# Kernel tuning notes

Measured on AMD Instinct MI355X. Metric: run time of the kernel, lower is better.

## Reference

```python
import math
import jax, jax.numpy as jnp
import numpy as np

FS = 16000          # sample rate implied by undefined global `fs` in source
NFFT = 320          # win_len == frame_len
HOP = 160           # inc
C_SOUND = 340.0
ARRAY_DIS = 0.027


def _steering(F, n_ch, angle_deg):
    # h = conj(exp(-1j*2*pi*f_k * sensor * d * sin(theta)/c)) -> exp(+1j*...)
    f_k = np.arange(F) * (FS // NFFT)                      # integer bins * 50 Hz
    delay = np.arange(n_ch) * ARRAY_DIS * np.sin(angle_deg * np.pi / 180.0) / C_SOUND
    h = np.exp(1j * 2.0 * np.pi * f_k[:, None] * delay[None, :]).astype(np.complex64)
    return jnp.asarray(h)[..., None]                       # [F, C, 1]


def _stft(x, window):
    # x: [B, C, L] float32; torch.stft defaults: center=True, reflect pad
    pad = NFFT // 2
    xp = jnp.pad(x, ((0, 0), (0, 0), (pad, pad)), mode='reflect')
    T = 1 + (xp.shape[-1] - NFFT) // HOP
    idx = jnp.arange(T)[:, None] * HOP + jnp.arange(NFFT)[None, :]
    frames = xp[:, :, idx] * window                        # [B, C, T, NFFT]
    return jnp.fft.rfft(frames, axis=-1)                   # [B, C, T, F] complex64


def _istft(S):
    # S: [B, F, T] complex; torch.istft with default (rectangular) window
    frames = jnp.fft.irfft(jnp.moveaxis(S, 1, 2), n=NFFT, axis=-1)  # [B, T, NFFT]
    B, T, _ = frames.shape
    out_len = NFFT + HOP * (T - 1)
    idx = jnp.arange(T)[:, None] * HOP + jnp.arange(NFFT)[None, :]
    out = jnp.zeros((B, out_len), frames.dtype).at[:, idx].add(frames)
    wsum = jnp.zeros((out_len,), frames.dtype).at[idx.reshape(-1)].add(1.0)
    pad = NFFT // 2
    return (out / wsum)[:, pad:-pad]


def setup_inputs() -> dict:
    key = jax.random.key(0)
    B, L, C = 8, 160000, 4
    mc_wav = jax.random.normal(key, (B, L, C), dtype=jnp.float32)
    # torch.kaiser_window(320, periodic=True, beta=6)
    window = jnp.asarray(np.kaiser(NFFT + 1, 6.0)[:NFFT].astype(np.float32))
    return {"mc_wav": mc_wav, "window": window}


def reference(mc_wav, window):
    B, L, C = mc_wav.shape
    # pre-normalize: remove DC per channel, scale by per-batch global max-abs
    x = mc_wav - jnp.mean(mc_wav, axis=1, keepdims=True)
    x = x / jnp.max(jnp.abs(x), axis=(1, 2), keepdims=True)
    x = jnp.transpose(x, (0, 2, 1))                        # [B, C, L]

    S = _stft(x, window)                                   # [B, C, T, F]
    F = S.shape[-1]
    Xs = jnp.transpose(S, (2, 0, 3, 1))                    # [T, B, F, C] frames-first
    T = Xs.shape[0]

    h1 = _steering(F, C, -40.0)                            # [F, C, 1]
    h2 = _steering(F, C, 40.0)
    eye = jnp.eye(C, dtype=S.dtype)

    def beam(invR, h, X):
        num = jnp.einsum('bfcd,fdo->bfco', invR, h)        # invR @ h  [B,F,C,1]
        den = jnp.einsum('fco,bfco->bf', h.conj(), num)    # h^H invR h
        w = num[..., 0] / den[..., None]                   # [B, F, C]
        return jnp.einsum('bfc,bfc->bf', w.conj(), X)      # w^H X

    def step(RXX, inp):
        X, first = inp                                     # X: [B, F, C]
        outer = jnp.einsum('bfc,bfd->bfcd', X, X.conj())
        RXX = jnp.where(first, outer, 0.05 * RXX + 0.95 * outer)
        tr = jnp.trace(RXX, axis1=-2, axis2=-1)[..., None, None]
        invR = jnp.linalg.inv(RXX + (tr / C) * eye)        # diag-loaded inverse
        return RXX, (beam(invR, h1, X), beam(invR, h2, X))

    RXX0 = jnp.zeros((B, F, C, C), dtype=S.dtype)
    firsts = jnp.arange(T) == 0
    _, (s1, s2) = jax.lax.scan(step, RXX0, (Xs, firsts))

    S1 = jnp.transpose(s1, (1, 2, 0))                      # [B, F, T]
    S2 = jnp.transpose(s2, (1, 2, 0))
    return _istft(S1), _istft(S2)
```

## Files before the change

kernel.cpp:

```cpp
#include <hip/hip_runtime.h>
#include <hip/hip_bf16.h>
#include <math.h>

#define BB 8
#define LL 160000
#define CC 4
#define NFFT 320
#define HOP 160
#define FB 161
#define TT 1001
#define TP 1024
#define RBLK 128
#define PI_D 3.14159265358979323846
#define NPAD 160320

#define CH 2
#define SCH 504
#define KWARM 4

#define GM 16016
#define KSEC 352
#define LDK 704
#define KT 11

typedef __attribute__((ext_vector_type(8))) short bf16x8;
typedef __attribute__((ext_vector_type(4))) float f32x4;

__device__ __forceinline__ float2 cmulf(float2 a, float2 b){
    return make_float2(a.x*b.x - a.y*b.y, a.x*b.y + a.y*b.x);
}
__device__ __forceinline__ float2 cmulcj(float2 a, float2 b){
    return make_float2(a.x*b.x + a.y*b.y, a.y*b.x - a.x*b.y);
}
__device__ __forceinline__ float2 cjmul(float2 a, float2 b){
    return make_float2(a.x*b.x + a.y*b.y, a.x*b.y - a.y*b.x);
}
__device__ __forceinline__ float2 csub(float2 a, float2 b){ return make_float2(a.x-b.x, a.y-b.y); }
__device__ __forceinline__ float2 cscale(float2 a, float s){ return make_float2(a.x*s, a.y*s); }
__device__ __forceinline__ float2 cdivf(float2 a, float2 b){
    float inv = 1.0f/(b.x*b.x + b.y*b.y);
    return make_float2((a.x*b.x + a.y*b.y)*inv, (a.y*b.x - a.x*b.y)*inv);
}
__device__ __forceinline__ short bf_hi(float v){
    __hip_bfloat16 h = __float2bfloat16(v);
    short s; __builtin_memcpy(&s, &h, 2); return s;
}
__device__ __forceinline__ short bf_lo(float v){
    __hip_bfloat16 h = __float2bfloat16(v);
    float r = v - __bfloat162float(h);
    __hip_bfloat16 l = __float2bfloat16(r);
    short s; __builtin_memcpy(&s, &l, 2); return s;
}

__global__ void k_gen(const float* __restrict__ win, float* __restrict__ htab,
                      short* __restrict__ Bts, short* __restrict__ Bt){
    int gid = blockIdx.x*256 + threadIdx.x;
    if (gid < 2*FB*CC){
        int i = gid;
        int c = i & 3;
        int k = (i >> 2) % FB;
        int m = i / (FB*CC);
        double coef = 2.0*PI_D*50.0*0.027*sin(40.0*PI_D/180.0)/340.0;
        double sgn = (m == 0) ? -1.0 : 1.0;
        double ph = sgn*coef*(double)k*(double)c;
        double s, c2;
        sincos(ph, &s, &c2);
        ((float2*)htab)[i] = make_float2((float)c2, (float)s);
        return;
    }
    gid -= 2*FB*CC;
    if (gid < 384*640){
        int col = gid / 640, kk = gid % 640;
        int n = (kk >= 320) ? kk - 320 : kk;
        int sec = (kk >= 320) ? 1 : 0;
        float v = 0.f;
        if (col < 2*FB){
            int k = col >> 1;
            double th = 2.0*PI_D*(double)k*(double)n/320.0;
            double s, co; sincos(th, &s, &co);
            double tw = (col & 1) ? -s : co;
            v = (float)((double)win[n]*tw);
        }
        Bts[gid] = sec ? bf_lo(v) : bf_hi(v);
        return;
    }
    gid -= 384*640;
    if (gid < NFFT*LDK){
        int n = gid / LDK, kk = gid % LDK;
        int sec = (kk >= KSEC) ? 1 : 0;
        int kk2 = kk - (sec ? KSEC : 0);
        float v = 0.f;
        if (kk2 < 2*FB){
            int bin = kk2 >> 1;
            double c = ((bin == 0 || bin == 160) ? 1.0 : 2.0) / 320.0;
            double th = 2.0*PI_D*(double)bin*(double)n/320.0;
            double s, co; sincos(th, &s, &co);
            v = (float)((kk2 & 1) ? -c*s : c*co);
        }
        Bt[(size_t)n*LDK + kk] = sec ? bf_lo(v) : bf_hi(v);
    }
}

__global__ __launch_bounds__(256) void k_stats1(const float* __restrict__ in, float* __restrict__ part){
    __shared__ float4 s4[256];
    __shared__ float4 mn4[256];
    __shared__ float4 mx4[256];
    int b = blockIdx.x / RBLK, chunk = blockIdx.x % RBLK;
    int tid = threadIdx.x;
    const float4* p = (const float4*)(in + (size_t)b*LL*CC);
    const int per = LL / RBLK;
    int start = chunk*per;
    float4 s  = make_float4(0.f,0.f,0.f,0.f);
    float4 mn = make_float4( 3.4e38f, 3.4e38f, 3.4e38f, 3.4e38f);
    float4 mx = make_float4(-3.4e38f,-3.4e38f,-3.4e38f,-3.4e38f);
    for (int i = start + tid; i < start + per; i += 256){
        float4 v = p[i];
        s.x += v.x; s.y += v.y; s.z += v.z; s.w += v.w;
        mn.x = fminf(mn.x, v.x); mn.y = fminf(mn.y, v.y); mn.z = fminf(mn.z, v.z); mn.w = fminf(mn.w, v.w);
        mx.x = fmaxf(mx.x, v.x); mx.y = fmaxf(mx.y, v.y); mx.z = fmaxf(mx.z, v.z); mx.w = fmaxf(mx.w, v.w);
    }
    s4[tid] = s; mn4[tid] = mn; mx4[tid] = mx;
    __syncthreads();
    for (int st = 128; st >= 1; st >>= 1){
        if (tid < st){
            float4 a = s4[tid], c = s4[tid+st];
            s4[tid] = make_float4(a.x+c.x, a.y+c.y, a.z+c.z, a.w+c.w);
            float4 d = mn4[tid], e = mn4[tid+st];
            mn4[tid] = make_float4(fminf(d.x,e.x), fminf(d.y,e.y), fminf(d.z,e.z), fminf(d.w,e.w));
            float4 f = mx4[tid], g = mx4[tid+st];
            mx4[tid] = make_float4(fmaxf(f.x,g.x), fmaxf(f.y,g.y), fmaxf(f.z,g.z), fmaxf(f.w,g.w));
        }
        __syncthreads();
    }
    if (tid == 0){
        float* dst = part + (size_t)(b*RBLK + chunk)*12;
        float4 a = s4[0], d = mn4[0], f = mx4[0];
        dst[0]=a.x; dst[1]=a.y; dst[2]=a.z; dst[3]=a.w;
        dst[4]=d.x; dst[5]=d.y; dst[6]=d.z; dst[7]=d.w;
        dst[8]=f.x; dst[9]=f.y; dst[10]=f.z; dst[11]=f.w;
    }
}

__global__ __launch_bounds__(128) void k_stats2(const float* __restrict__ part,
                                                float* __restrict__ mean, float* __restrict__ invmax){
    __shared__ float4 s4[128];
    __shared__ float4 mn4[128];
    __shared__ float4 mx4[128];
    int b = blockIdx.x, tid = threadIdx.x;
    const float* src = part + (size_t)(b*RBLK + tid)*12;
    s4[tid]  = make_float4(src[0], src[1], src[2], src[3]);
    mn4[tid] = make_float4(src[4], src[5], src[6], src[7]);
    mx4[tid] = make_float4(src[8], src[9], src[10], src[11]);
    __syncthreads();
    for (int st = 64; st >= 1; st >>= 1){
        if (tid < st){
            float4 a = s4[tid], c = s4[tid+st];
            s4[tid] = make_float4(a.x+c.x, a.y+c.y, a.z+c.z, a.w+c.w);
            float4 d = mn4[tid], e = mn4[tid+st];
            mn4[tid] = make_float4(fminf(d.x,e.x), fminf(d.y,e.y), fminf(d.z,e.z), fminf(d.w,e.w));
            float4 f = mx4[tid], g = mx4[tid+st];
            mx4[tid] = make_float4(fmaxf(f.x,g.x), fmaxf(f.y,g.y), fmaxf(f.z,g.z), fmaxf(f.w,g.w));
        }
        __syncthreads();
    }
    if (tid == 0){
        float4 sum = s4[0], mn = mn4[0], mx = mx4[0];
        float m0 = sum.x*(1.0f/LL), m1 = sum.y*(1.0f/LL), m2 = sum.z*(1.0f/LL), m3 = sum.w*(1.0f/LL);
        mean[b*4+0]=m0; mean[b*4+1]=m1; mean[b*4+2]=m2; mean[b*4+3]=m3;
        float a0 = fmaxf(mx.x - m0, m0 - mn.x);
        float a1 = fmaxf(mx.y - m1, m1 - mn.y);
        float a2 = fmaxf(mx.z - m2, m2 - mn.z);
        float a3 = fmaxf(mx.w - m3, m3 - mn.w);
        invmax[b] = 1.0f / fmaxf(fmaxf(a0, a1), fmaxf(a2, a3));
    }
}

__global__ __launch_bounds__(256) void k_anorm(const float* __restrict__ in,
        const float* __restrict__ mean, const float* __restrict__ invmax,
        short* __restrict__ Ahi, short* __restrict__ Alo){
    int gid = blockIdx.x*256 + threadIdx.x;
    if (gid >= BB*CC*(NPAD/8)) return;
    int p8 = gid % (NPAD/8);
    int bc = gid / (NPAD/8);
    int b = bc >> 2;
    float mc = mean[bc];
    float iv = invmax[b];
    const float* px = in + (size_t)b*LL*CC + (bc & 3);
    bf16x8 h8, l8;
    #pragma unroll
    for (int j = 0; j < 8; ++j){
        int p = p8*8 + j - 160;
        int m2 = p < 0 ? -p : (p >= LL ? 2*LL - 2 - p : p);
        float v = (px[(size_t)m2*CC] - mc) * iv;
        __hip_bfloat16 h = __float2bfloat16(v);
        float r = v - __bfloat162float(h);
        __hip_bfloat16 l = __float2bfloat16(r);
        short hs, ls; __builtin_memcpy(&hs, &h, 2); __builtin_memcpy(&ls, &l, 2);
        h8[j] = hs; l8[j] = ls;
    }
    size_t o = (size_t)bc*NPAD + (size_t)p8*8;
    *(bf16x8*)&Ahi[o] = h8;
    *(bf16x8*)&Alo[o] = l8;
}

__global__ __launch_bounds__(256) void k_gstft(const short* __restrict__ Ahi, const short* __restrict__ Alo,
        const short* __restrict__ Bts, float* __restrict__ S){
    __shared__ short stage[4*2560];
    short* Ah = stage;
    short* Al = stage + 2560;
    short* Bh = stage + 5120;
    short* Bl = stage + 7680;
    float* Ct = (float*)stage;
    int tid = threadIdx.x;
    int row0 = blockIdx.x*64;
    int col0 = blockIdx.y*64;
    int b  = row0 >> 12;
    int t0 = (row0 & 4095) >> 2;
    int tr = tid >> 2, tq = tid & 3, tk = tq*8;
    int tloc = t0 + (tr >> 2);
    int c    = tr & 3;
    bool vt  = tloc < TT;
    const short* pah = Ahi + (size_t)(b*4 + c)*NPAD;
    const short* pal = Alo + (size_t)(b*4 + c)*NPAD;
    int npbase = tloc*160;
    int wave = tid >> 6, lane = tid & 63;
    int wm = wave >> 1, wn = wave & 1;
    int l15 = lane & 15, quad = lane >> 4;
    f32x4 acc00 = {0.f,0.f,0.f,0.f}, acc01 = acc00, acc10 = acc00, acc11 = acc00;
    for (int kt = 0; kt < 10; ++kt){
        int k0 = kt*32;
        __syncthreads();
        bf16x8 hv = {}, lv = {};
        if (vt){
            hv = *(const bf16x8*)&pah[npbase + k0 + tk];
            lv = *(const bf16x8*)&pal[npbase + k0 + tk];
        }
        *(bf16x8*)&Ah[tr*40 + tk] = hv;
        *(bf16x8*)&Al[tr*40 + tk] = lv;
        const short* bp = Bts + (size_t)(col0 + tr)*640 + k0 + tk;
        *(bf16x8*)&Bh[tr*40 + tk] = *(const bf16x8*)bp;
        *(bf16x8*)&Bl[tr*40 + tk] = *(const bf16x8*)(bp + 320);
        __syncthreads();
        bf16x8 a0h = *(bf16x8*)&Ah[(wm*32 + l15)*40 + quad*8];
        bf16x8 a1h = *(bf16x8*)&Ah[(wm*32 + 16 + l15)*40 + quad*8];
        bf16x8 a0l = *(bf16x8*)&Al[(wm*32 + l15)*40 + quad*8];
        bf16x8 a1l = *(bf16x8*)&Al[(wm*32 + 16 + l15)*40 + quad*8];
        bf16x8 b0h = *(bf16x8*)&Bh[(wn*32 + l15)*40 + quad*8];
        bf16x8 b1h = *(bf16x8*)&Bh[(wn*32 + 16 + l15)*40 + quad*8];
        bf16x8 b0l = *(bf16x8*)&Bl[(wn*32 + l15)*40 + quad*8];
        bf16x8 b1l = *(bf16x8*)&Bl[(wn*32 + 16 + l15)*40 + quad*8];
        acc00 = __builtin_amdgcn_mfma_f32_16x16x32_bf16(a0h, b0h, acc00, 0, 0, 0);
        acc01 = __builtin_amdgcn_mfma_f32_16x16x32_bf16(a0h, b1h, acc01, 0, 0, 0);
        acc10 = __builtin_amdgcn_mfma_f32_16x16x32_bf16(a1h, b0h, acc10, 0, 0, 0);
        acc11 = __builtin_amdgcn_mfma_f32_16x16x32_bf16(a1h, b1h, acc11, 0, 0, 0);
        acc00 = __builtin_amdgcn_mfma_f32_16x16x32_bf16(a0l, b0h, acc00, 0, 0, 0);
        acc01 = __builtin_amdgcn_mfma_f32_16x16x32_bf16(a0l, b1h, acc01, 0, 0, 0);
        acc10 = __builtin_amdgcn_mfma_f32_16x16x32_bf16(a1l, b0h, acc10, 0, 0, 0);
        acc11 = __builtin_amdgcn_mfma_f32_16x16x32_bf16(a1l, b1h, acc11, 0, 0, 0);
        acc00 = __builtin_amdgcn_mfma_f32_16x16x32_bf16(a0h, b0l, acc00, 0, 0, 0);
        acc01 = __builtin_amdgcn_mfma_f32_16x16x32_bf16(a0h, b1l, acc01, 0, 0, 0);
        acc10 = __builtin_amdgcn_mfma_f32_16x16x32_bf16(a1h, b0l, acc10, 0, 0, 0);
        acc11 = __builtin_amdgcn_mfma_f32_16x16x32_bf16(a1h, b1l, acc11, 0, 0, 0);
    }
    __syncthreads();
    #pragma unroll
    for (int r = 0; r < 4; ++r){
        int rl = wm*32 + quad*4 + r;
        Ct[rl*66 + wn*32 + l15]           = acc00[r];
        Ct[rl*66 + wn*32 + l15 + 16]      = acc01[r];
        Ct[(rl+16)*66 + wn*32 + l15]      = acc10[r];
        Ct[(rl+16)*66 + wn*32 + l15 + 16] = acc11[r];
    }
    __syncthreads();
    int tl = tid & 15, h = (tid >> 4) & 1, kq = tid >> 5;
    int t = t0 + tl;
    if (t < TT){
        float4* S4 = (float4*)S;
        for (int kk = kq; kk < 32; kk += 8){
            int kg = (col0 >> 1) + kk;
            if (kg < FB){
                float2 e0 = *(float2*)&Ct[(tl*4 + 2*h)*66 + 2*kk];
                float2 e1 = *(float2*)&Ct[(tl*4 + 2*h + 1)*66 + 2*kk];
                S4[((size_t)(b*FB + kg)*TT + t)*2 + h] = make_float4(e0.x, e0.y, e1.x, e1.y);
            }
        }
    }
}

#define UPD(first) do{ \
    float aa = (first) ? 0.f : 0.05f; float wg = (first) ? 1.f : 0.95f; \
    float y0x=wg*x0.x, y0y=wg*x0.y, y1x=wg*x1.x, y1y=wg*x1.y; \
    float y2x=wg*x2.x, y2y=wg*x2.y, y3x=wg*x3.x, y3y=wg*x3.y; \
    d0 = aa*d0 + y0x*x0.x + y0y*x0.y; \
    d1 = aa*d1 + y1x*x1.x + y1y*x1.y; \
    d2 = aa*d2 + y2x*x2.x + y2y*x2.y; \
    d3 = aa*d3 + y3x*x3.x + y3y*x3.y; \
    r10.x = aa*r10.x + y1x*x0.x + y1y*x0.y;  r10.y = aa*r10.y + y1y*x0.x - y1x*x0.y; \
    r20.x = aa*r20.x + y2x*x0.x + y2y*x0.y;  r20.y = aa*r20.y + y2y*x0.x - y2x*x0.y; \
    r30.x = aa*r30.x + y3x*x0.x + y3y*x0.y;  r30.y = aa*r30.y + y3y*x0.x - y3x*x0.y; \
    r21.x = aa*r21.x + y2x*x1.x + y2y*x1.y;  r21.y = aa*r21.y + y2y*x1.x - y2x*x1.y; \
    r31.x = aa*r31.x + y3x*x1.x + y3y*x1.y;  r31.y = aa*r31.y + y3y*x1.x - y3x*x1.y; \
    r32.x = aa*r32.x + y3x*x2.x + y3y*x2.y;  r32.y = aa*r32.y + y3y*x2.x - y3x*x2.y; \
}while(0)

__global__ __launch_bounds__(256) void k_scan(const float* __restrict__ S, const float* __restrict__ htab,
                      float* __restrict__ S1, float* __restrict__ S2){
    __shared__ float4 tile[1008];
    int bid = blockIdx.x;
    int half = bid & 1;
    int bf = bid >> 1;
    int f  = bf % FB;
    int tid = threadIdx.x;
    int tbase = half*SCH;
    int te  = tbase + SCH; if (te > TT) te = TT;
    int nst = 2*(te - tbase);
    const float4* Sg = (const float4*)S + (size_t)bf*TT*2;
    const float4* Sp = Sg + (size_t)tbase*2;
    for (int i = tid; i < nst; i += 256)
        tile[i ^ ((i>>4)&7)] = Sp[i];
    __syncthreads();
    float2 out1[CH], out2[CH];
    int t0 = tbase + tid*CH;
    bool act = (tid*CH < SCH) && (t0 < TT);
    if (act){
        const float2* hp = (const float2*)htab;
        float2 ha0 = hp[f*4+0], ha1 = hp[f*4+1], ha2 = hp[f*4+2], ha3 = hp[f*4+3];
        float2 hb0 = hp[(FB+f)*4+0], hb1 = hp[(FB+f)*4+1], hb2 = hp[(FB+f)*4+2], hb3 = hp[(FB+f)*4+3];
        float d0=0,d1=0,d2=0,d3=0;
        float2 r10={0,0}, r20={0,0}, r30={0,0}, r21={0,0}, r31={0,0}, r32={0,0};
        int ts = t0 - KWARM; if (ts < 0) ts = 0;
        for (int tau = ts; tau < t0; ++tau){
            float4 v0, v1;
            if (tau >= tbase){
                int i0 = 2*(tau - tbase);
                v0 = tile[i0 ^ ((i0>>4)&7)];
                v1 = tile[(i0+1) ^ ((i0>>4)&7)];
            } else {
                v0 = Sg[2*tau];
                v1 = Sg[2*tau + 1];
            }
            float2 x0 = make_float2(v0.x, v0.y), x1 = make_float2(v0.z, v0.w);
            float2 x2 = make_float2(v1.x, v1.y), x3 = make_float2(v1.z, v1.w);
            UPD(tau == 0);
        }
        for (int j = 0; j < CH; ++j){
            int t = t0 + j;
            if (t >= TT) break;
            int i0 = 2*(t - tbase);
            float4 v0 = tile[i0 ^ ((i0>>4)&7)];
            float4 v1 = tile[(i0+1) ^ ((i0>>4)&7)];
            float2 x0 = make_float2(v0.x, v0.y), x1 = make_float2(v0.z, v0.w);
            float2 x2 = make_float2(v1.x, v1.y), x3 = make_float2(v1.z, v1.w);
            UPD(t == 0);
            float trc = d0 + d1 + d2 + d3;
            float lam = trc * 0.25f;
            float e0 = d0 + lam, e1 = d1 + lam, e2 = d2 + lam, e3 = d3 + lam;
            float detP = e0*e1 - (r10.x*r10.x + r10.y*r10.y);
            float2 w00 = csub(cscale(r20, e1), cmulf(r10, r21));
            float2 w01 = csub(cscale(r30, e1), cmulf(r10, r31));
            float2 w10 = csub(cscale(r21, e0), cjmul(r10, r20));
            float2 w11 = csub(cscale(r31, e0), cjmul(r10, r30));
            float2 va = cjmul(r30, w00), vb = cjmul(r31, w10);
            float2 V10 = make_float2(va.x + vb.x, -(va.y + vb.y));
            float reV00 = r20.x*w00.x + r20.y*w00.y + r21.x*w10.x + r21.y*w10.y;
            float reV11 = r30.x*w01.x + r30.y*w01.y + r31.x*w11.x + r31.y*w11.y;
            float t00 = detP*e2 - reV00;
            float t11 = detP*e3 - reV11;
            float2 t10 = csub(cscale(r32, detP), V10);
            float detT = t00*t11 - (t10.x*t10.x + t10.y*t10.y);
            #pragma unroll
            for (int m = 0; m < 2; ++m){
                float2 h0 = m ? hb0 : ha0;
                float2 h1 = m ? hb1 : ha1;
                float2 h2 = m ? hb2 : ha2;
                float2 h3 = m ? hb3 : ha3;
                float2 g0 = csub(cscale(h0, e1), cjmul(r10, h1));
                float2 g1 = csub(cscale(h1, e0), cmulf(r10, h0));
                float2 ta = cmulf(r20, g0), tb = cmulf(r21, g1);
                float2 hh0 = make_float2(detP*h2.x - ta.x - tb.x, detP*h2.y - ta.y - tb.y);
                ta = cmulf(r30, g0); tb = cmulf(r31, g1);
                float2 hh1 = make_float2(detP*h3.x - ta.x - tb.x, detP*h3.y - ta.y - tb.y);
                float2 y20 = csub(cscale(hh0, t11), cjmul(t10, hh1));
                float2 y21 = csub(cscale(hh1, t00), cmulf(t10, hh0));
                float2 u20 = cscale(y20, detP), u21 = cscale(y21, detP);
                ta = cmulcj(y20, r20); tb = cmulcj(y21, r30);
                float2 q0 = make_float2(detT*h0.x - ta.x - tb.x, detT*h0.y - ta.y - tb.y);
                ta = cmulcj(y20, r21); tb = cmulcj(y21, r31);
                float2 q1 = make_float2(detT*h1.x - ta.x - tb.x, detT*h1.y - ta.y - tb.y);
                float2 u10 = csub(cscale(q0, e1), cjmul(r10, q1));
                float2 u11 = csub(cscale(q1, e0), cmulf(r10, q0));
                float2 den = cjmul(h0, u10), tmp;
                tmp = cjmul(h1, u11); den.x += tmp.x; den.y += tmp.y;
                tmp = cjmul(h2, u20); den.x += tmp.x; den.y += tmp.y;
                tmp = cjmul(h3, u21); den.x += tmp.x; den.y += tmp.y;
                float2 num = cjmul(u10, x0);
                tmp = cjmul(u11, x1); num.x += tmp.x; num.y += tmp.y;
                tmp = cjmul(u20, x2); num.x += tmp.x; num.y += tmp.y;
                tmp = cjmul(u21, x3); num.x += tmp.x; num.y += tmp.y;
                float2 s = cdivf(num, make_float2(den.x, -den.y));
                if (m) out2[j] = s; else out1[j] = s;
            }
        }
    }
    __syncthreads();
    float2* o1 = (float2*)tile;
    float2* o2 = ((float2*)tile) + 528;
    if (act){
        for (int j = 0; j < CH && t0 + j < TT; ++j){
            int lt = t0 - tbase + j;
            int iw = lt ^ ((lt>>3)&7);
            o1[iw] = out1[j];
            o2[iw] = out2[j];
        }
    }
    __syncthreads();
    int nout = te - tbase;
    float2* S1g = (float2*)S1 + (size_t)bf*TT + tbase;
    float2* S2g = (float2*)S2 + (size_t)bf*TT + tbase;
    for (int i = tid; i < nout; i += 256){
        int ir = i ^ ((i>>3)&7);
        S1g[i] = o1[ir];
        S2g[i] = o2[ir];
    }
}

__global__ __launch_bounds__(256) void k_pack(const float* __restrict__ S1, const float* __restrict__ S2,
                                              short* __restrict__ A){
    __shared__ short tile[32*708];
    int bid = blockIdx.x;
    int tb = bid & 31, rb = bid >> 5;
    int t0 = tb*32;
    int beam = rb >> 3, b = rb & 7;
    const float2* Sp = (const float2*)(beam ? S2 : S1) + (size_t)b*FB*TT;
    int tid = threadIdx.x;
    for (int idx = tid; idx < 32*176; idx += 256){
        int bin = idx >> 5, tq = idx & 31;
        int t = t0 + tq;
        float2 s = make_float2(0.f, 0.f);
        if (bin < FB && t < TT) s = Sp[(size_t)bin*TT + t];
        int c0 = 2*bin;
        tile[tq*708 + c0]            = bf_hi(s.x);
        tile[tq*708 + c0 + 1]        = bf_hi(s.y);
        tile[tq*708 + KSEC + c0]     = bf_lo(s.x);
        tile[tq*708 + KSEC + c0 + 1] = bf_lo(s.y);
    }
    __syncthreads();
    for (int idx = tid; idx < 32*176; idx += 256){
        int tq = idx / 176, k4 = idx % 176;
        int t = t0 + tq;
        if (t < TT)
            *(short4*)&A[(size_t)(rb*TT + t)*LDK + k4*4] = *(short4*)&tile[tq*708 + k4*4];
    }
}

__global__ __launch_bounds__(256) void k_gemm(const short* __restrict__ A, const short* __restrict__ Bt,
                                              float* __restrict__ C){
    __shared__ short As[64*40];
    __shared__ short Bs[64*40];
    int tid = threadIdx.x;
    int row0 = blockIdx.x * 64;
    int col0 = blockIdx.y * 64;
    int wave = tid >> 6, lane = tid & 63;
    int wm = wave >> 1, wn = wave & 1;
    int l15 = lane & 15, quad = lane >> 4;
    f32x4 acc00 = {0.f,0.f,0.f,0.f}, acc01 = acc00, acc10 = acc00, acc11 = acc00;
    int tr = tid >> 2;
    int tk = (tid & 3) * 8;
    int gr = row0 + tr;
    bool rok = gr < GM;
    const size_t arow = (size_t)gr*LDK;
    const size_t brow = (size_t)(col0 + tr)*LDK;
    for (int seg = 0; seg < 3; ++seg){
        int aofs = (seg == 1) ? KSEC : 0;
        int bofs = (seg == 2) ? KSEC : 0;
        for (int kt = 0; kt < KT; ++kt){
            int k0 = kt*32;
            __syncthreads();
            bf16x8 av = {};
            if (rok) av = *(const bf16x8*)&A[arow + aofs + k0 + tk];
            bf16x8 bv = *(const bf16x8*)&Bt[brow + bofs + k0 + tk];
            *(bf16x8*)&As[tr*40 + tk] = av;
            *(bf16x8*)&Bs[tr*40 + tk] = bv;
            __syncthreads();
            bf16x8 a0 = *(bf16x8*)&As[(wm*32 + l15)*40 + quad*8];
            bf16x8 a1 = *(bf16x8*)&As[(wm*32 + 16 + l15)*40 + quad*8];
            bf16x8 b0 = *(bf16x8*)&Bs[(wn*32 + l15)*40 + quad*8];
            bf16x8 b1 = *(bf16x8*)&Bs[(wn*32 + 16 + l15)*40 + quad*8];
            acc00 = __builtin_amdgcn_mfma_f32_16x16x32_bf16(a0, b0, acc00, 0, 0, 0);
            acc01 = __builtin_amdgcn_mfma_f32_16x16x32_bf16(a0, b1, acc01, 0, 0, 0);
            acc10 = __builtin_amdgcn_mfma_f32_16x16x32_bf16(a1, b0, acc10, 0, 0, 0);
            acc11 = __builtin_amdgcn_mfma_f32_16x16x32_bf16(a1, b1, acc11, 0, 0, 0);
        }
    }
    for (int r = 0; r < 4; ++r){
        int orow0 = row0 + wm*32 + quad*4 + r;
        int ocol0 = col0 + wn*32 + l15;
        if (orow0 < GM){
            C[(size_t)orow0*NFFT + ocol0]      = acc00[r];
            C[(size_t)orow0*NFFT + ocol0 + 16] = acc01[r];
        }
        if (orow0 + 16 < GM){
            C[(size_t)(orow0+16)*NFFT + ocol0]      = acc10[r];
            C[(size_t)(orow0+16)*NFFT + ocol0 + 16] = acc11[r];
        }
    }
}

__global__ __launch_bounds__(256) void k_ola(const float* __restrict__ frames, float* __restrict__ out){
    int gid = blockIdx.x*256 + threadIdx.x;
    if (gid >= 2*BB*(LL/4)) return;
    int o4 = (gid % (LL/4))*4;
    int rb = gid / (LL/4);
    int i  = o4 + HOP;
    int t1 = i / HOP;
    int r  = i - t1*HOP;
    const float4* fb = (const float4*)(frames + (size_t)rb*TT*NFFT);
    float4 a = fb[(t1*NFFT + r) >> 2];
    float4 b = fb[((t1-1)*NFFT + r + HOP) >> 2];
    ((float4*)out)[gid] = make_float4(0.5f*(a.x+b.x), 0.5f*(a.y+b.y), 0.5f*(a.z+b.z), 0.5f*(a.w+b.w));
}

extern "C" void kernel_launch(void* const* d_in, const int* in_sizes, int n_in,
                              void* d_out, int out_size, void* d_ws, size_t ws_size,
                              hipStream_t stream){
    const float* in  = (const float*)d_in[0];
    const float* win = (const float*)d_in[1];
    float* ws = (float*)d_ws;
    float* mean   = ws;
    float* invmax = ws + 32;
    float* htab   = ws + 48;
    float* S1     = ws + 3072;
    size_t nS1 = (size_t)2*BB*FB*TT;
    float* S2 = S1 + nS1;
    float* S  = S2 + nS1;
    float* part = S1;
    short* Ahi = (short*)S1;
    short* Alo = Ahi + (size_t)BB*CC*NPAD;
    short* Bts = (short*)d_out;
    short* Bt  = (short*)((float*)d_out + 131072);
    short* A  = (short*)S;
    float* frames = S1;

    int ngen = 2*FB*CC + 384*640 + NFFT*LDK;
    k_gen<<<dim3((ngen + 255)/256), dim3(256), 0, stream>>>(win, htab, Bts, Bt);
    k_stats1<<<dim3(BB*RBLK), dim3(256), 0, stream>>>(in, part);
    k_stats2<<<dim3(BB), dim3(128), 0, stream>>>(part, mean, invmax);
    k_anorm<<<dim3((BB*CC*(NPAD/8) + 255)/256), dim3(256), 0, stream>>>(in, mean, invmax, Ahi, Alo);
    k_gstft<<<dim3(BB*TP*CC/64, 6), dim3(256), 0, stream>>>(Ahi, Alo, Bts, S);
    k_scan<<<dim3(2*BB*FB), dim3(256), 0, stream>>>(S, htab, S1, S2);
    k_pack<<<dim3(512), dim3(256), 0, stream>>>(S1, S2, A);
    k_gemm<<<dim3((GM + 63)/64, NFFT/64), dim3(256), 0, stream>>>(A, Bt, frames);
    k_ola<<<dim3((2*BB*(LL/4) + 255)/256), dim3(256), 0, stream>>>(frames, (float*)d_out);
}
```

Baseline: 223.4 us.

## Load MFMA operands directly from global memory, dropping LDS staging in GEMMs

Both the STFT GEMM and the inverse-transform GEMM stop staging A/B tiles through shared memory with two barriers per k-step. Each wave now loads its MFMA fragments straight from global memory, with row indices clamped instead of predicated and the k-loops partially unrolled. This removes the barriers and LDS round trips, but each wave duplicates global loads that were shared before, so it relies on L1/L2 hits. Out-of-range rows now read a clamped valid row rather than zeros; only valid outputs are stored.

New measurement: 311.7 us. 1.4x slower.

```diff
diff --git a/kernel.cpp b/kernel.cpp
--- a/kernel.cpp
+++ b/kernel.cpp
@@ -205,50 +205,40 @@
 
 __global__ __launch_bounds__(256) void k_gstft(const short* __restrict__ Ahi, const short* __restrict__ Alo,
         const short* __restrict__ Bts, float* __restrict__ S){
-    __shared__ short stage[4*2560];
-    short* Ah = stage;
-    short* Al = stage + 2560;
-    short* Bh = stage + 5120;
-    short* Bl = stage + 7680;
-    float* Ct = (float*)stage;
+    __shared__ float Ct[64*66];
     int tid = threadIdx.x;
     int row0 = blockIdx.x*64;
     int col0 = blockIdx.y*64;
     int b  = row0 >> 12;
     int t0 = (row0 & 4095) >> 2;
-    int tr = tid >> 2, tq = tid & 3, tk = tq*8;
-    int tloc = t0 + (tr >> 2);
-    int c    = tr & 3;
-    bool vt  = tloc < TT;
-    const short* pah = Ahi + (size_t)(b*4 + c)*NPAD;
-    const short* pal = Alo + (size_t)(b*4 + c)*NPAD;
-    int npbase = tloc*160;
+    if (t0 >= TT) return;
     int wave = tid >> 6, lane = tid & 63;
     int wm = wave >> 1, wn = wave & 1;
     int l15 = lane & 15, quad = lane >> 4;
+    int r0 = wm*32 + l15;
+    int r1 = r0 + 16;
+    int tl0 = t0 + (r0 >> 2); if (tl0 >= TT) tl0 = TT - 1;
+    int tl1 = t0 + (r1 >> 2); if (tl1 >= TT) tl1 = TT - 1;
+    size_t oa0 = (size_t)(b*4 + (r0 & 3))*NPAD + (size_t)tl0*160 + quad*8;
+    size_t oa1 = (size_t)(b*4 + (r1 & 3))*NPAD + (size_t)tl1*160 + quad*8;
+    const short* pa0h = Ahi + oa0;
+    const short* pa0l = Alo + oa0;
+    const short* pa1h = Ahi + oa1;
+    const short* pa1l = Alo + oa1;
+    const short* pb0 = Bts + (size_t)(col0 + wn*32 + l15)*640 + quad*8;
+    const short* pb1 = Bts + (size_t)(col0 + wn*32 + 16 + l15)*640 + quad*8;
     f32x4 acc00 = {0.f,0.f,0.f,0.f}, acc01 = acc00, acc10 = acc00, acc11 = acc00;
+    #pragma unroll 2
     for (int kt = 0; kt < 10; ++kt){
         int k0 = kt*32;
-        __syncthreads();
-        bf16x8 hv = {}, lv = {};
-        if (vt){
-            hv = *(const bf16x8*)&pah[npbase + k0 + tk];
-            lv = *(const bf16x8*)&pal[npbase + k0 + tk];
-        }
-        *(bf16x8*)&Ah[tr*40 + tk] = hv;
-        *(bf16x8*)&Al[tr*40 + tk] = lv;
-        const short* bp = Bts + (size_t)(col0 + tr)*640 + k0 + tk;
-        *(bf16x8*)&Bh[tr*40 + tk] = *(const bf16x8*)bp;
-        *(bf16x8*)&Bl[tr*40 + tk] = *(const bf16x8*)(bp + 320);
-        __syncthreads();
-        bf16x8 a0h = *(bf16x8*)&Ah[(wm*32 + l15)*40 + quad*8];
-        bf16x8 a1h = *(bf16x8*)&Ah[(wm*32 + 16 + l15)*40 + quad*8];
-        bf16x8 a0l = *(bf16x8*)&Al[(wm*32 + l15)*40 + quad*8];
-        bf16x8 a1l = *(bf16x8*)&Al[(wm*32 + 16 + l15)*40 + quad*8];
-        bf16x8 b0h = *(bf16x8*)&Bh[(wn*32 + l15)*40 + quad*8];
-        bf16x8 b1h = *(bf16x8*)&Bh[(wn*32 + 16 + l15)*40 + quad*8];
-        bf16x8 b0l = *(bf16x8*)&Bl[(wn*32 + l15)*40 + quad*8];
-        bf16x8 b1l = *(bf16x8*)&Bl[(wn*32 + 16 + l15)*40 + quad*8];
+        bf16x8 a0h = *(const bf16x8*)(pa0h + k0);
+        bf16x8 a1h = *(const bf16x8*)(pa1h + k0);
+        bf16x8 a0l = *(const bf16x8*)(pa0l + k0);
+        bf16x8 a1l = *(const bf16x8*)(pa1l + k0);
+        bf16x8 b0h = *(const bf16x8*)(pb0 + k0);
+        bf16x8 b1h = *(const bf16x8*)(pb1 + k0);
+        bf16x8 b0l = *(const bf16x8*)(pb0 + 320 + k0);
+        bf16x8 b1l = *(const bf16x8*)(pb1 + 320 + k0);
         acc00 = __builtin_amdgcn_mfma_f32_16x16x32_bf16(a0h, b0h, acc00, 0, 0, 0);
         acc01 = __builtin_amdgcn_mfma_f32_16x16x32_bf16(a0h, b1h, acc01, 0, 0, 0);
         acc10 = __builtin_amdgcn_mfma_f32_16x16x32_bf16(a1h, b0h, acc10, 0, 0, 0);
@@ -262,7 +252,6 @@
         acc10 = __builtin_amdgcn_mfma_f32_16x16x32_bf16(a1h, b0l, acc10, 0, 0, 0);
         acc11 = __builtin_amdgcn_mfma_f32_16x16x32_bf16(a1h, b1l, acc11, 0, 0, 0);
     }
-    __syncthreads();
     #pragma unroll
     for (int r = 0; r < 4; ++r){
         int rl = wm*32 + quad*4 + r;
@@ -455,37 +444,31 @@
 
 __global__ __launch_bounds__(256) void k_gemm(const short* __restrict__ A, const short* __restrict__ Bt,
                                               float* __restrict__ C){
-    __shared__ short As[64*40];
-    __shared__ short Bs[64*40];
     int tid = threadIdx.x;
     int row0 = blockIdx.x * 64;
     int col0 = blockIdx.y * 64;
     int wave = tid >> 6, lane = tid & 63;
     int wm = wave >> 1, wn = wave & 1;
     int l15 = lane & 15, quad = lane >> 4;
+    int gr0 = row0 + wm*32 + l15;      if (gr0 >= GM) gr0 = GM - 1;
+    int gr1 = row0 + wm*32 + 16 + l15; if (gr1 >= GM) gr1 = GM - 1;
+    const short* pa0 = A + (size_t)gr0*LDK + quad*8;
+    const short* pa1 = A + (size_t)gr1*LDK + quad*8;
+    const short* pb0 = Bt + (size_t)(col0 + wn*32 + l15)*LDK + quad*8;
+    const short* pb1 = Bt + (size_t)(col0 + wn*32 + 16 + l15)*LDK + quad*8;
     f32x4 acc00 = {0.f,0.f,0.f,0.f}, acc01 = acc00, acc10 = acc00, acc11 = acc00;
-    int tr = tid >> 2;
-    int tk = (tid & 3) * 8;
-    int gr = row0 + tr;
-    bool rok = gr < GM;
-    const size_t arow = (size_t)gr*LDK;
-    const size_t brow = (size_t)(col0 + tr)*LDK;
+    #pragma unroll
     for (int seg = 0; seg < 3; ++seg){
         int aofs = (seg == 1) ? KSEC : 0;
         int bofs = (seg == 2) ? KSEC : 0;
+        #pragma unroll 2
         for (int kt = 0; kt < KT; ++kt){
-            int k0 = kt*32;
-            __syncthreads();
-            bf16x8 av = {};
-            if (rok) av = *(const bf16x8*)&A[arow + aofs + k0 + tk];
-            bf16x8 bv = *(const bf16x8*)&Bt[brow + bofs + k0 + tk];
-            *(bf16x8*)&As[tr*40 + tk] = av;
-            *(bf16x8*)&Bs[tr*40 + tk] = bv;
-            __syncthreads();
-            bf16x8 a0 = *(bf16x8*)&As[(wm*32 + l15)*40 + quad*8];
-            bf16x8 a1 = *(bf16x8*)&As[(wm*32 + 16 + l15)*40 + quad*8];
-            bf16x8 b0 = *(bf16x8*)&Bs[(wn*32 + l15)*40 + quad*8];
-            bf16x8 b1 = *(bf16x8*)&Bs[(wn*32 + 16 + l15)*40 + quad*8];
+            int ka = aofs + kt*32;
+            int kb = bofs + kt*32;
+            bf16x8 a0 = *(const bf16x8*)(pa0 + ka);
+            bf16x8 a1 = *(const bf16x8*)(pa1 + ka);
+            bf16x8 b0 = *(const bf16x8*)(pb0 + kb);
+            bf16x8 b1 = *(const bf16x8*)(pb1 + kb);
             acc00 = __builtin_amdgcn_mfma_f32_16x16x32_bf16(a0, b0, acc00, 0, 0, 0);
             acc01 = __builtin_amdgcn_mfma_f32_16x16x32_bf16(a0, b1, acc01, 0, 0, 0);
             acc10 = __builtin_amdgcn_mfma_f32_16x16x32_bf16(a1, b0, acc10, 0, 0, 0);
```
